# Kernel tuning notes

Hardware: AMD Instinct MI355X
Metric: run time of the kernel (lower is better)

The kernel has to match this reference:

```python
import jax, jax.numpy as jnp
import numpy as np

B = 8      # number of drug-target pairs in the packed batch
NR = 3200  # total packed residues
NA = 320   # total packed atoms
TD = 512   # target (GearNet) feature dim
DD = 128   # drug (EGNN) feature dim
H = 128    # hidden_dim


def setup_inputs() -> dict:
    key = jax.random.key(0)
    ks = jax.random.split(key, 10)
    seg_res = jnp.sort(jax.random.randint(ks[0], (NR,), 0, B, dtype=jnp.int32))
    seg_atom = jnp.sort(jax.random.randint(ks[1], (NA,), 0, B, dtype=jnp.int32))
    return {
        "target_feature": jax.random.normal(ks[2], (NR, TD), jnp.float32),
        "drug_feature": jax.random.normal(ks[3], (NA, DD), jnp.float32),
        "target_pos": jax.random.normal(ks[4], (NR, 3), jnp.float32) * 10.0,
        "drug_pos": jax.random.normal(ks[5], (NA, 3), jnp.float32) * 10.0,
        "Wt": jax.random.normal(ks[6], (TD, H), jnp.float32) / np.sqrt(TD).astype(np.float32),
        "bt": jnp.zeros((H,), jnp.float32),
        "Wd": jax.random.normal(ks[7], (DD, H), jnp.float32) / np.sqrt(DD).astype(np.float32),
        "bd": jnp.zeros((H,), jnp.float32),
        "seg_res": seg_res,
        "seg_atom": seg_atom,
    }


def reference(target_feature, drug_feature, target_pos, drug_pos, Wt, bt, Wd, bd, seg_res, seg_atom):
    # Linear projections (torchdrug MLP with a single hidden dim == plain Linear)
    tf = target_feature @ Wt + bt  # [NR, H]
    df = drug_feature @ Wd + bd    # [NA, H]

    # Block-diagonal mask: pair (i, j) is valid iff residue i and atom j belong
    # to the same DT-pair (replaces the Python loop that zeroes cross blocks).
    mask = seg_res[:, None] == seg_atom[None, :]  # [NR, NA]

    # Pairwise residue-atom distances
    D = jnp.linalg.norm(target_pos[:, None, :] - drug_pos[None, :, :], axis=-1)  # [NR, NA]

    # Per-block min/max distance (min/max over the masked block only)
    row_min = jnp.min(jnp.where(mask, D, jnp.inf), axis=1)   # [NR]
    row_max = jnp.max(jnp.where(mask, D, -jnp.inf), axis=1)  # [NR]
    dmin = jax.ops.segment_min(row_min, seg_res, num_segments=B)  # [B]
    dmax = jax.ops.segment_max(row_max, seg_res, num_segments=B)  # [B]
    dmin = jnp.where(jnp.isfinite(dmin), dmin, 0.0)
    dmax = jnp.where(jnp.isfinite(dmax), dmax, 1.0)
    denom = jnp.where(dmax > dmin, dmax - dmin, 1.0)

    # Normalized distance inside blocks, zero outside (matches the torch loop)
    dnorm = jnp.where(mask, (D - dmin[seg_res][:, None]) / denom[seg_res][:, None], 0.0)

    # Feature difference inside blocks, zero outside
    imap = jnp.where(mask[:, :, None], tf[:, None, :] - df[None, :, :], 0.0)  # [NR, NA, H]

    # scaled=False -> no 1/sqrt(hidden_dim) scaling
    return jnp.tanh(imap + dnorm[:, :, None])
```

## Files before the change

### kernel.cpp

```cpp
#include <hip/hip_runtime.h>
#include <math.h>

constexpr int NR = 3200;
constexpr int NA = 320;
constexpr int TD = 512;
constexpr int DD = 128;
constexpr int H  = 128;
constexpr int B  = 8;
constexpr int NP = NR * NA;

constexpr int ROWS_T = 4;
constexpr int ROWS_D = 8;
constexpr int NBLK_T = NR / ROWS_T;
constexpr int NBLK_D = NA / ROWS_D;

typedef float f4 __attribute__((ext_vector_type(4)));

__global__ __launch_bounds__(256) void mega_kernel(
    const float* __restrict__ At, const float* __restrict__ Wt, const float* __restrict__ bt,
    const float* __restrict__ Ad, const float* __restrict__ Wd, const float* __restrict__ bd,
    const float* __restrict__ tpos, const float* __restrict__ dpos,
    const int* __restrict__ seg_res, const int* __restrict__ seg_atom,
    float* __restrict__ tf, float* __restrict__ df,
    float* __restrict__ Dbuf, float* __restrict__ rowmin, float* __restrict__ rowmax) {
    __shared__ float sA[ROWS_T * TD];
    __shared__ float sAcc[ROWS_D * H];
    const int b = blockIdx.x;
    const int t = threadIdx.x;

    if (b < NBLK_T) {
        const int h = t & (H - 1), half = t >> 7, i0 = b * ROWS_T;
        for (int idx = t; idx < ROWS_T * TD; idx += 256)
            sA[idx] = At[i0 * TD + idx];
        __syncthreads();
        float acc[ROWS_T];
#pragma unroll
        for (int r = 0; r < ROWS_T; r++) acc[r] = 0.0f;
        const int k0 = half * (TD / 2), k1 = k0 + (TD / 2);
#pragma unroll 4
        for (int k = k0; k < k1; k++) {
            const float w = Wt[k * H + h];
#pragma unroll
            for (int r = 0; r < ROWS_T; r++)
                acc[r] = fmaf(sA[r * TD + k], w, acc[r]);
        }
        if (half) {
#pragma unroll
            for (int r = 0; r < ROWS_T; r++) sAcc[r * H + h] = acc[r];
        }
        __syncthreads();
        if (!half) {
            const float bv = bt[h];
#pragma unroll
            for (int r = 0; r < ROWS_T; r++)
                tf[(i0 + r) * H + h] = acc[r] + sAcc[r * H + h] + bv;
        }
    } else if (b < NBLK_T + NBLK_D) {
        const int h = t & (H - 1), half = t >> 7, i0 = (b - NBLK_T) * ROWS_D;
        for (int idx = t; idx < ROWS_D * DD; idx += 256)
            sA[idx] = Ad[i0 * DD + idx];
        __syncthreads();
        float acc[ROWS_D];
#pragma unroll
        for (int r = 0; r < ROWS_D; r++) acc[r] = 0.0f;
        const int k0 = half * (DD / 2), k1 = k0 + (DD / 2);
#pragma unroll 4
        for (int k = k0; k < k1; k++) {
            const float w = Wd[k * H + h];
#pragma unroll
            for (int r = 0; r < ROWS_D; r++)
                acc[r] = fmaf(sA[r * DD + k], w, acc[r]);
        }
        if (half) {
#pragma unroll
            for (int r = 0; r < ROWS_D; r++) sAcc[r * H + h] = acc[r];
        }
        __syncthreads();
        if (!half) {
            const float bv = bd[h];
#pragma unroll
            for (int r = 0; r < ROWS_D; r++)
                df[(i0 + r) * H + h] = acc[r] + sAcc[r * H + h] + bv;
        }
    } else {
        const int i  = b - NBLK_T - NBLK_D;
        const int sr = seg_res[i];
        const float tx = tpos[3 * i], ty = tpos[3 * i + 1], tz = tpos[3 * i + 2];
        float vmin = INFINITY, vmax = -INFINITY;
        for (int j = t; j < NA; j += 256) {
            const float dx = tx - dpos[3 * j];
            const float dy = ty - dpos[3 * j + 1];
            const float dz = tz - dpos[3 * j + 2];
            const float d  = sqrtf(dx * dx + dy * dy + dz * dz);
            Dbuf[i * NA + j] = d;
            if (seg_atom[j] == sr) {
                vmin = fminf(vmin, d);
                vmax = fmaxf(vmax, d);
            }
        }
#pragma unroll
        for (int off = 32; off > 0; off >>= 1) {
            vmin = fminf(vmin, __shfl_down(vmin, off));
            vmax = fmaxf(vmax, __shfl_down(vmax, off));
        }
        const int wid = t >> 6, lane = t & 63;
        if (lane == 0) { sAcc[wid] = vmin; sAcc[4 + wid] = vmax; }
        __syncthreads();
        if (t == 0) {
            float mn = sAcc[0], mx = sAcc[4];
#pragma unroll
            for (int w = 1; w < 4; w++) {
                mn = fminf(mn, sAcc[w]);
                mx = fmaxf(mx, sAcc[4 + w]);
            }
            rowmin[i] = mn;
            rowmax[i] = mx;
        }
    }
}

__global__ __launch_bounds__(512) void segreduce_kernel(
    const float* __restrict__ rowmin, const float* __restrict__ rowmax,
    const int* __restrict__ seg_res, float2* __restrict__ params) {
    const int s    = threadIdx.x >> 6;
    const int lane = threadIdx.x & 63;
    float mn = INFINITY, mx = -INFINITY;
    for (int r = lane; r < NR; r += 64) {
        if (seg_res[r] == s) {
            mn = fminf(mn, rowmin[r]);
            mx = fmaxf(mx, rowmax[r]);
        }
    }
#pragma unroll
    for (int off = 32; off > 0; off >>= 1) {
        mn = fminf(mn, __shfl_down(mn, off));
        mx = fmaxf(mx, __shfl_down(mx, off));
    }
    if (lane == 0) {
        const float dmin = (mn < INFINITY)  ? mn : 0.0f;
        const float dmax = (mx > -INFINITY) ? mx : 1.0f;
        const float denom = (dmax > dmin) ? (dmax - dmin) : 1.0f;
        params[s] = make_float2(dmin, 1.0f / denom);
    }
}

__device__ __forceinline__ float fast_tanh(float x) {
    const float cx = fminf(fmaxf(x, -15.0f), 15.0f);
    const float e  = __expf(2.0f * cx);
    return 1.0f - __fdividef(2.0f, e + 1.0f);
}

__global__ __launch_bounds__(256) void final_kernel(
    const float* __restrict__ tf, const float* __restrict__ df,
    const float* __restrict__ Dbuf,
    const int* __restrict__ seg_res, const int* __restrict__ seg_atom,
    const float2* __restrict__ params, float* __restrict__ out) {
    const int i = blockIdx.y;
    const int e = (blockIdx.x * 256 + threadIdx.x) * 4;
    const int j = e >> 7;
    const int h = e & 127;

    f4 o = {0.0f, 0.0f, 0.0f, 0.0f};
    const int sr = seg_res[i];
    if (seg_atom[j] == sr) {
        const float2 pp = params[sr];
        const float  dn = (Dbuf[i * NA + j] - pp.x) * pp.y;
        const f4 tv = *(const f4*)(tf + i * H + h);
        const f4 dv = *(const f4*)(df + j * H + h);
        o.x = fast_tanh(tv.x - dv.x + dn);
        o.y = fast_tanh(tv.y - dv.y + dn);
        o.z = fast_tanh(tv.z - dv.z + dn);
        o.w = fast_tanh(tv.w - dv.w + dn);
    }
    __builtin_nontemporal_store(o, (f4*)(out + (long long)i * (NA * H) + e));
}

extern "C" void kernel_launch(void* const* d_in, const int* in_sizes, int n_in,
                              void* d_out, int out_size, void* d_ws, size_t ws_size,
                              hipStream_t stream) {
    const float* target_feature = (const float*)d_in[0];
    const float* drug_feature   = (const float*)d_in[1];
    const float* target_pos     = (const float*)d_in[2];
    const float* drug_pos       = (const float*)d_in[3];
    const float* Wt             = (const float*)d_in[4];
    const float* bt             = (const float*)d_in[5];
    const float* Wd             = (const float*)d_in[6];
    const float* bd             = (const float*)d_in[7];
    const int*   seg_res        = (const int*)d_in[8];
    const int*   seg_atom       = (const int*)d_in[9];
    float* out = (float*)d_out;

    float* ws     = (float*)d_ws;
    float* tf     = ws;
    float* df     = tf + NR * H;
    float* Dbuf   = df + NA * H;
    float* rowmin = Dbuf + NP;
    float* rowmax = rowmin + NR;
    float2* params = (float2*)(rowmax + NR);

    mega_kernel<<<NBLK_T + NBLK_D + NR, 256, 0, stream>>>(
        target_feature, Wt, bt, drug_feature, Wd, bd,
        target_pos, drug_pos, seg_res, seg_atom, tf, df, Dbuf, rowmin, rowmax);
    segreduce_kernel<<<1, 512, 0, stream>>>(rowmin, rowmax, seg_res, params);
    final_kernel<<<dim3(NA * H / (4 * 256), NR), 256, 0, stream>>>(
        tf, df, Dbuf, seg_res, seg_atom, params, out);
}
```

Measured before the change: 564.0 us.

## Compute per-segment min/max directly on sorted segments and recompute distances in final kernel

The full NR x NA distance buffer and the separate segment-reduce kernel are removed. Per-segment ranges are found by counting the sorted segment ids, and each segment's min/max is reduced over its own diagonal block using squared distances, with sqrt applied once at the end. The final kernel recomputes each distance from the positions instead of reading the stored buffer. This removes a 4 MB write and read plus one launch, at the cost of redundant sqrt work in the final kernel and a reliance on the segment ids being sorted.

```diff
diff --git a/kernel.cpp b/kernel.cpp
--- a/kernel.cpp
+++ b/kernel.cpp
@@ -7,7 +7,6 @@
 constexpr int DD = 128;
 constexpr int H  = 128;
 constexpr int B  = 8;
-constexpr int NP = NR * NA;
 
 constexpr int ROWS_T = 4;
 constexpr int ROWS_D = 8;
@@ -16,15 +15,15 @@
 
 typedef float f4 __attribute__((ext_vector_type(4)));
 
-__global__ __launch_bounds__(256) void mega_kernel(
+__global__ __launch_bounds__(256) void prep_kernel(
     const float* __restrict__ At, const float* __restrict__ Wt, const float* __restrict__ bt,
     const float* __restrict__ Ad, const float* __restrict__ Wd, const float* __restrict__ bd,
     const float* __restrict__ tpos, const float* __restrict__ dpos,
     const int* __restrict__ seg_res, const int* __restrict__ seg_atom,
-    float* __restrict__ tf, float* __restrict__ df,
-    float* __restrict__ Dbuf, float* __restrict__ rowmin, float* __restrict__ rowmax) {
+    float* __restrict__ tf, float* __restrict__ df, float2* __restrict__ params) {
     __shared__ float sA[ROWS_T * TD];
     __shared__ float sAcc[ROWS_D * H];
+    __shared__ int   sI[16];
     const int b = blockIdx.x;
     const int t = threadIdx.x;
 
@@ -83,64 +82,56 @@
                 df[(i0 + r) * H + h] = acc[r] + sAcc[r * H + h] + bv;
         }
     } else {
-        const int i  = b - NBLK_T - NBLK_D;
-        const int sr = seg_res[i];
-        const float tx = tpos[3 * i], ty = tpos[3 * i + 1], tz = tpos[3 * i + 2];
-        float vmin = INFINITY, vmax = -INFINITY;
-        for (int j = t; j < NA; j += 256) {
-            const float dx = tx - dpos[3 * j];
-            const float dy = ty - dpos[3 * j + 1];
-            const float dz = tz - dpos[3 * j + 2];
-            const float d  = sqrtf(dx * dx + dy * dy + dz * dz);
-            Dbuf[i * NA + j] = d;
-            if (seg_atom[j] == sr) {
-                vmin = fminf(vmin, d);
-                vmax = fmaxf(vmax, d);
+        const int s    = b - NBLK_T - NBLK_D;
+        const int lane = t & 63, wid = t >> 6;
+        int c0 = 0, c1 = 0, c2 = 0, c3 = 0;
+        for (int r = t; r < NR; r += 256) {
+            const int v = seg_res[r];
+            c0 += (v < s); c1 += (v <= s);
+        }
+        for (int a = t; a < NA; a += 256) {
+            const int v = seg_atom[a];
+            c2 += (v < s); c3 += (v <= s);
+        }
+#pragma unroll
+        for (int off = 32; off > 0; off >>= 1) {
+            c0 += __shfl_down(c0, off); c1 += __shfl_down(c1, off);
+            c2 += __shfl_down(c2, off); c3 += __shfl_down(c3, off);
+        }
+        if (lane == 0) { sI[wid] = c0; sI[4 + wid] = c1; sI[8 + wid] = c2; sI[12 + wid] = c3; }
+        __syncthreads();
+        const int r0 = sI[0] + sI[1] + sI[2] + sI[3];
+        const int r1 = sI[4] + sI[5] + sI[6] + sI[7];
+        const int a0 = sI[8] + sI[9] + sI[10] + sI[11];
+        const int a1 = sI[12] + sI[13] + sI[14] + sI[15];
+        float mn = INFINITY, mx = -INFINITY;
+        for (int i = r0 + wid; i < r1; i += 4) {
+            const float tx = tpos[3 * i], ty = tpos[3 * i + 1], tz = tpos[3 * i + 2];
+            for (int j = a0 + lane; j < a1; j += 64) {
+                const float dx = tx - dpos[3 * j];
+                const float dy = ty - dpos[3 * j + 1];
+                const float dz = tz - dpos[3 * j + 2];
+                const float d2 = fmaf(dx, dx, fmaf(dy, dy, dz * dz));
+                mn = fminf(mn, d2);
+                mx = fmaxf(mx, d2);
             }
         }
 #pragma unroll
         for (int off = 32; off > 0; off >>= 1) {
-            vmin = fminf(vmin, __shfl_down(vmin, off));
-            vmax = fmaxf(vmax, __shfl_down(vmax, off));
+            mn = fminf(mn, __shfl_down(mn, off));
+            mx = fmaxf(mx, __shfl_down(mx, off));
         }
-        const int wid = t >> 6, lane = t & 63;
-        if (lane == 0) { sAcc[wid] = vmin; sAcc[4 + wid] = vmax; }
+        __syncthreads();
+        if (lane == 0) { sAcc[wid] = mn; sAcc[4 + wid] = mx; }
         __syncthreads();
         if (t == 0) {
-            float mn = sAcc[0], mx = sAcc[4];
-#pragma unroll
-            for (int w = 1; w < 4; w++) {
-                mn = fminf(mn, sAcc[w]);
-                mx = fmaxf(mx, sAcc[4 + w]);
-            }
-            rowmin[i] = mn;
-            rowmax[i] = mx;
+            const float m2 = fminf(fminf(sAcc[0], sAcc[1]), fminf(sAcc[2], sAcc[3]));
+            const float x2 = fmaxf(fmaxf(sAcc[4], sAcc[5]), fmaxf(sAcc[6], sAcc[7]));
+            const float dmin  = (m2 < INFINITY)  ? sqrtf(m2) : 0.0f;
+            const float dmax  = (x2 > -INFINITY) ? sqrtf(x2) : 1.0f;
+            const float denom = (dmax > dmin) ? (dmax - dmin) : 1.0f;
+            params[s] = make_float2(dmin, 1.0f / denom);
         }
-    }
-}
-
-__global__ __launch_bounds__(512) void segreduce_kernel(
-    const float* __restrict__ rowmin, const float* __restrict__ rowmax,
-    const int* __restrict__ seg_res, float2* __restrict__ params) {
-    const int s    = threadIdx.x >> 6;
-    const int lane = threadIdx.x & 63;
-    float mn = INFINITY, mx = -INFINITY;
-    for (int r = lane; r < NR; r += 64) {
-        if (seg_res[r] == s) {
-            mn = fminf(mn, rowmin[r]);
-            mx = fmaxf(mx, rowmax[r]);
-        }
-    }
-#pragma unroll
-    for (int off = 32; off > 0; off >>= 1) {
-        mn = fminf(mn, __shfl_down(mn, off));
-        mx = fmaxf(mx, __shfl_down(mx, off));
-    }
-    if (lane == 0) {
-        const float dmin = (mn < INFINITY)  ? mn : 0.0f;
-        const float dmax = (mx > -INFINITY) ? mx : 1.0f;
-        const float denom = (dmax > dmin) ? (dmax - dmin) : 1.0f;
-        params[s] = make_float2(dmin, 1.0f / denom);
     }
 }
 
@@ -152,7 +143,7 @@
 
 __global__ __launch_bounds__(256) void final_kernel(
     const float* __restrict__ tf, const float* __restrict__ df,
-    const float* __restrict__ Dbuf,
+    const float* __restrict__ tpos, const float* __restrict__ dpos,
     const int* __restrict__ seg_res, const int* __restrict__ seg_atom,
     const float2* __restrict__ params, float* __restrict__ out) {
     const int i = blockIdx.y;
@@ -164,7 +155,11 @@
     const int sr = seg_res[i];
     if (seg_atom[j] == sr) {
         const float2 pp = params[sr];
-        const float  dn = (Dbuf[i * NA + j] - pp.x) * pp.y;
+        const float dx = tpos[3 * i]     - dpos[3 * j];
+        const float dy = tpos[3 * i + 1] - dpos[3 * j + 1];
+        const float dz = tpos[3 * i + 2] - dpos[3 * j + 2];
+        const float d  = sqrtf(fmaf(dx, dx, fmaf(dy, dy, dz * dz)));
+        const float dn = (d - pp.x) * pp.y;
         const f4 tv = *(const f4*)(tf + i * H + h);
         const f4 dv = *(const f4*)(df + j * H + h);
         o.x = fast_tanh(tv.x - dv.x + dn);
@@ -190,18 +185,14 @@
     const int*   seg_atom       = (const int*)d_in[9];
     float* out = (float*)d_out;
 
-    float* ws     = (float*)d_ws;
-    float* tf     = ws;
-    float* df     = tf + NR * H;
-    float* Dbuf   = df + NA * H;
-    float* rowmin = Dbuf + NP;
-    float* rowmax = rowmin + NR;
-    float2* params = (float2*)(rowmax + NR);
+    float*  ws     = (float*)d_ws;
+    float*  tf     = ws;
+    float*  df     = tf + NR * H;
+    float2* params = (float2*)(df + NA * H);
 
-    mega_kernel<<<NBLK_T + NBLK_D + NR, 256, 0, stream>>>(
+    prep_kernel<<<NBLK_T + NBLK_D + B, 256, 0, stream>>>(
         target_feature, Wt, bt, drug_feature, Wd, bd,
-        target_pos, drug_pos, seg_res, seg_atom, tf, df, Dbuf, rowmin, rowmax);
-    segreduce_kernel<<<1, 512, 0, stream>>>(rowmin, rowmax, seg_res, params);
+        target_pos, drug_pos, seg_res, seg_atom, tf, df, params);
     final_kernel<<<dim3(NA * H / (4 * 256), NR), 256, 0, stream>>>(
-        tf, df, Dbuf, seg_res, seg_atom, params, out);
+        tf, df, target_pos, drug_pos, seg_res, seg_atom, params, out);
 }
```

Measured after the change: 565.1 us. No clear change (+0.2%).
